# Kernel optimization log

Hardware: AMD Instinct MI355X
Metric: run time of the kernel (lower is better)

Reference implementation:

```python
import jax, jax.numpy as jnp
import numpy as np

N, NH, D, REP, C, SUB = 512, 32, 1024, 1024, 16, 64
GAMA, EPS, LN_EPS = 0.9, 1e-10, 1e-5
IMG_H, IMG_W = 800, 1280


def spatial_enc(b1, b2, h, w):
    # pocket.ops.compute_spatial_encodings: 18 handcrafted pair features + their logs -> 36
    c1x = (b1[:, 0] + b1[:, 2]) * 0.5; c1y = (b1[:, 1] + b1[:, 3]) * 0.5
    c2x = (b2[:, 0] + b2[:, 2]) * 0.5; c2y = (b2[:, 1] + b2[:, 3]) * 0.5
    b1w = b1[:, 2] - b1[:, 0]; b1h = b1[:, 3] - b1[:, 1]
    b2w = b2[:, 2] - b2[:, 0]; b2h = b2[:, 3] - b2[:, 1]
    dx = jnp.abs(c2x - c1x) / (b1w + EPS)
    dy = jnp.abs(c2y - c1y) / (b1h + EPS)
    ltx = jnp.maximum(b1[:, 0], b2[:, 0]); lty = jnp.maximum(b1[:, 1], b2[:, 1])
    rbx = jnp.minimum(b1[:, 2], b2[:, 2]); rby = jnp.minimum(b1[:, 3], b2[:, 3])
    inter = jnp.clip(rbx - ltx, 0.0) * jnp.clip(rby - lty, 0.0)
    a1 = b1w * b1h; a2 = b2w * b2h
    iou = inter / (a1 + a2 - inter)
    f = jnp.stack([
        c1x / w, c1y / h, c2x / w, c2y / h,
        b1w / w, b1h / h, b2w / w, b2h / h,
        a1 / (h * w), a2 / (h * w), a2 / (a1 + EPS),
        b1w / (b1h + EPS), b2w / (b2h + EPS), iou,
        (c2x > c1x) * dx, (c2x < c1x) * dx,
        (c2y > c1y) * dy, (c2y < c1y) * dy,
    ], axis=1)
    return jnp.concatenate([f, jnp.log(f + EPS)], axis=1)


def mbf(a, s, w1, b1, w2, b2, w3, b3):
    # relu(sum_c fc3_c(relu(fc1_c(a) * fc2_c(s)))) with branches batched over c
    u1 = jnp.einsum('pd,cdk->cpk', a, w1) + b1[:, None, :]
    u2 = jnp.einsum('ps,csk->cpk', s, w2) + b2[:, None, :]
    hdn = jax.nn.relu(u1 * u2)  # [C,P,SUB]
    out = jnp.einsum('cpk,cko->po', hdn, w3) + b3.sum(0)
    return jax.nn.relu(out)


def ln(x, g, b):
    m = x.mean(-1, keepdims=True)
    v = ((x - m) ** 2).mean(-1, keepdims=True)
    return (x - m) / jnp.sqrt(v + LN_EPS) * g + b


def setup_inputs():
    key = jax.random.key(0)
    ks = jax.random.split(key, 16)
    labels = jnp.where(jnp.arange(N) < NH, 0, 1).astype(jnp.int32)  # first NH nodes are humans
    node = jax.random.normal(ks[0], (N, D), jnp.float32)
    cx = jax.random.uniform(ks[1], (N,)) * (IMG_W * 0.5)
    cy = jax.random.uniform(ks[2], (N,)) * (IMG_H * 0.5)
    bw = jax.random.uniform(ks[3], (N,)) * (IMG_W * 0.3) + 8.0
    bh = jax.random.uniform(ks[4], (N,)) * (IMG_H * 0.3) + 8.0
    coords = jnp.stack([cx, cy, cx + bw, cy + bh], axis=1)
    p = lambda k, shp: jax.random.normal(k, shp, jnp.float32) * 0.02
    return dict(
        labels=labels, node=node, coords=coords, image_h=IMG_H, image_w=IMG_W,
        sp_w1=p(ks[5], (36, 128)), sp_b1=jnp.zeros(128),
        sp_w2=p(ks[6], (128, 256)), sp_b2=jnp.zeros(256),
        sp_w3=p(ks[7], (256, 1024)), sp_b3=jnp.zeros(1024),
        att_w1=p(ks[8], (C, 2 * D, SUB)), att_b1=jnp.zeros((C, SUB)),
        att_w2=p(ks[9], (C, 1024, SUB)), att_b2=jnp.zeros((C, SUB)),
        att_w3=p(ks[10], (C, SUB, REP)), att_b3=jnp.zeros((C, REP)),
        adj_w=p(ks[11], (REP,)), adj_b=jnp.zeros(()),
        lnh_g=jnp.ones(D), lnh_b=jnp.zeros(D),
        lno_g=jnp.ones(D), lno_b=jnp.zeros(D),
    )


def reference(labels, node, coords, image_h, image_w,
              sp_w1, sp_b1, sp_w2, sp_b2, sp_w3, sp_b3,
              att_w1, att_b1, att_w2, att_b2, att_w3, att_b3,
              adj_w, adj_b, lnh_g, lnh_b, lno_g, lno_b):
    n = node.shape[0]
    n_h = int((np.asarray(labels) == 0).sum())
    xi = np.repeat(np.arange(n_h), n)  # human index per pair
    yj = np.tile(np.arange(n), n_h)    # node index per pair
    keep = np.nonzero(xi != yj)[0]
    x = jnp.asarray(xi); y = jnp.asarray(yj)
    x_keep = jnp.asarray(xi[keep]); y_keep = jnp.asarray(yj[keep])

    f = spatial_enc(coords[x], coords[y], float(image_h), float(image_w))  # [P,36]
    sp = jax.nn.relu(f @ sp_w1 + sp_b1)
    sp = jax.nn.relu(sp @ sp_w2 + sp_b2)
    sp = jax.nn.relu(sp @ sp_w3 + sp_b3)  # [P,1024]

    human_node = node[:n_h]
    adjacency = None
    for _ in range(2):  # num_iter
        a = jnp.concatenate([human_node[x], node[y]], axis=1)  # [P,2D]
        weight = mbf(a, sp, att_w1, att_b1, att_w2, att_b2, att_w3, att_b3)  # [P,REP]
        adjacency = jax.nn.relu(weight @ adj_w + adj_b).reshape(n_h, n)
        hn_msg = adjacency @ node          # einsum('yx,xa->ya', adj, node)
        nd_msg = adjacency.T @ human_node  # einsum('yx,xa->ya', adj.T, human)
        node = ln(node * GAMA + (1.0 - GAMA) * nd_msg, lno_g, lno_b)
        human_node = ln(human_node * GAMA + (1.0 - GAMA) * hn_msg, lnh_g, lnh_b)

    return (human_node[x_keep], node[y_keep], adjacency[x_keep, y_keep], x_keep, y_keep)
```

## Files before the change

kernel.cpp:

```cpp
#include <hip/hip_runtime.h>
#include <hip/hip_bf16.h>


typedef __attribute__((ext_vector_type(4))) float  f32x4;
typedef __attribute__((ext_vector_type(8))) __bf16 bf16x8;
typedef __attribute__((ext_vector_type(4))) __bf16 bf16x4;

#define FEPS 1e-10f
#define LNEPS 1e-5f
#define GAMA_F 0.9f

__device__ __forceinline__ void gload16(const void* g, void* l) {
  __builtin_amdgcn_global_load_lds(
      (const __attribute__((address_space(1))) void*)g,
      (__attribute__((address_space(3))) void*)l, 16, 0, 0);
}

__device__ __forceinline__ float read_dim(const void* p) {
  int iv = *(const int*)p;
  if (iv > 0 && iv < (1 << 20)) return (float)iv;
  return *(const float*)p;
}

__global__ void prep_mega(const float* __restrict__ w1, const float* __restrict__ w2,
                          const float* __restrict__ w3, const float* __restrict__ spw3,
                          const float* __restrict__ spw1, const float* __restrict__ spw2,
                          const float* __restrict__ b3,
                          const float* __restrict__ node_in,
                          const float* __restrict__ coords,
                          const void* __restrict__ imh, const void* __restrict__ imw,
                          __bf16* __restrict__ W1at, __bf16* __restrict__ W1bt,
                          __bf16* __restrict__ W2t, __bf16* __restrict__ W3t,
                          __bf16* __restrict__ SpW3t,
                          __bf16* __restrict__ SpW1t, __bf16* __restrict__ SpW2t,
                          float* __restrict__ b3s,
                          float* __restrict__ node_f, __bf16* __restrict__ node_b,
                          float* __restrict__ hn_f, __bf16* __restrict__ hn_b,
                          __bf16* __restrict__ f36) {
  __shared__ float tile[64][65];
  const int b = blockIdx.x, t = threadIdx.x;
  const int tc = t & 63, tr = t >> 6;
  if (b < 256) {
    const int c = b >> 4, d0 = (b & 15) << 6;
    #pragma unroll
    for (int pass = 0; pass < 2; ++pass) {
      const float* src = w1 + (size_t)c * 131072 + (size_t)(d0 + pass * 1024) * 64;
      __bf16* dst = pass ? W1bt : W1at;
      if (pass) __syncthreads();
      #pragma unroll
      for (int q = 0; q < 16; ++q) {
        int dd = q * 4 + tr;
        tile[dd][tc] = src[dd * 64 + tc];
      }
      __syncthreads();
      #pragma unroll
      for (int q = 0; q < 16; ++q) {
        int kk = q * 4 + tr;
        dst[(size_t)(c * 64 + kk) * 1024 + d0 + tc] = (__bf16)tile[tc][kk];
      }
    }
  } else if (b < 512) {
    const int bb = b - 256, c = bb >> 4, s0 = (bb & 15) << 6;
    const float* src = w2 + (size_t)c * 65536 + (size_t)s0 * 64;
    #pragma unroll
    for (int q = 0; q < 16; ++q) {
      int ss = q * 4 + tr;
      tile[ss][tc] = src[ss * 64 + tc];
    }
    __syncthreads();
    #pragma unroll
    for (int q = 0; q < 16; ++q) {
      int kk = q * 4 + tr;
      W2t[(size_t)(c * 64 + kk) * 1024 + s0 + tc] = (__bf16)tile[tc][kk];
    }
  } else if (b < 768) {
    const int bb = b - 512, c = bb >> 4, o0 = (bb & 15) << 6;
    const float* src = w3 + (size_t)c * 65536;
    #pragma unroll
    for (int q = 0; q < 16; ++q) {
      int kk = q * 4 + tr;
      tile[kk][tc] = src[kk * 1024 + o0 + tc];
    }
    __syncthreads();
    #pragma unroll
    for (int q = 0; q < 16; ++q) {
      int oo = q * 4 + tr;
      W3t[(size_t)(o0 + oo) * 1024 + c * 64 + tc] = (__bf16)tile[tc][oo];
    }
  } else if (b < 832) {
    const int bb = b - 768, o0 = (bb >> 2) << 6, k0 = (bb & 3) << 6;
    #pragma unroll
    for (int q = 0; q < 16; ++q) {
      int kk = q * 4 + tr;
      tile[kk][tc] = spw3[(size_t)(k0 + kk) * 1024 + o0 + tc];
    }
    __syncthreads();
    #pragma unroll
    for (int q = 0; q < 16; ++q) {
      int oo = q * 4 + tr;
      SpW3t[(size_t)(o0 + oo) * 256 + k0 + tc] = (__bf16)tile[tc][oo];
    }
  } else if (b < 960) {
    int gid = (b - 832) * 256 + t;
    if (gid < 8192) {
      int n = gid >> 6, k = gid & 63;
      SpW1t[gid] = (k < 36) ? (__bf16)spw1[k * 128 + n] : (__bf16)0.f;
    }
    {
      int n = gid >> 7, k = gid & 127;
      SpW2t[gid] = (__bf16)spw2[k * 256 + n];
    }
    if (gid < 1024) {
      float s = 0.f;
      for (int cc = 0; cc < 16; ++cc) s += b3[cc * 1024 + gid];
      b3s[gid] = s;
    }
  } else if (b < 3008) {
    int gid = (b - 960) * 256 + t;
    float v = node_in[gid];
    node_f[gid] = v;
    node_b[gid] = (__bf16)v;
    if (gid < 32 * 1024) { hn_f[gid] = v; hn_b[gid] = (__bf16)v; }
  } else {
    int p = (b - 3008) * 256 + t;
    int i = p >> 9, j = p & 511;
    float H = read_dim(imh), W = read_dim(imw);
    f32x4 b1 = ((const f32x4*)coords)[i];
    f32x4 b2 = ((const f32x4*)coords)[j];
    float c1x = (b1[0] + b1[2]) * 0.5f, c1y = (b1[1] + b1[3]) * 0.5f;
    float c2x = (b2[0] + b2[2]) * 0.5f, c2y = (b2[1] + b2[3]) * 0.5f;
    float b1w = b1[2] - b1[0], b1h = b1[3] - b1[1];
    float b2w = b2[2] - b2[0], b2h = b2[3] - b2[1];
    float dx = fabsf(c2x - c1x) / (b1w + FEPS);
    float dy = fabsf(c2y - c1y) / (b1h + FEPS);
    float ltx = fmaxf(b1[0], b2[0]), lty = fmaxf(b1[1], b2[1]);
    float rbx = fminf(b1[2], b2[2]), rby = fminf(b1[3], b2[3]);
    float inter = fmaxf(rbx - ltx, 0.f) * fmaxf(rby - lty, 0.f);
    float a1 = b1w * b1h, a2 = b2w * b2h;
    float iou = inter / (a1 + a2 - inter);
    float f[18];
    f[0] = c1x / W;  f[1] = c1y / H;  f[2] = c2x / W;  f[3] = c2y / H;
    f[4] = b1w / W;  f[5] = b1h / H;  f[6] = b2w / W;  f[7] = b2h / H;
    f[8] = a1 / (H * W); f[9] = a2 / (H * W); f[10] = a2 / (a1 + FEPS);
    f[11] = b1w / (b1h + FEPS); f[12] = b2w / (b2h + FEPS); f[13] = iou;
    f[14] = (c2x > c1x) ? dx : 0.f; f[15] = (c2x < c1x) ? dx : 0.f;
    f[16] = (c2y > c1y) ? dy : 0.f; f[17] = (c2y < c1y) ? dy : 0.f;
    __bf16 o[64];
    #pragma unroll
    for (int q = 0; q < 18; ++q) { o[q] = (__bf16)f[q]; o[18 + q] = (__bf16)logf(f[q] + FEPS); }
    #pragma unroll
    for (int q = 36; q < 64; ++q) o[q] = (__bf16)0.f;
    bf16x8* dst = (bf16x8*)(f36 + (size_t)p * 64);
    #pragma unroll
    for (int q = 0; q < 8; ++q) dst[q] = *(bf16x8*)&o[q * 8];
  }
}

__global__ __launch_bounds__(256)
void mlp_head(const __bf16* __restrict__ f36, const __bf16* __restrict__ SpW1t,
              const __bf16* __restrict__ SpW2t, const float* __restrict__ b1,
              const float* __restrict__ b2, __bf16* __restrict__ sp2out) {
  __shared__ __align__(16) __bf16 Af[128 * 64];
  __shared__ __align__(16) __bf16 W1s[128 * 64];
  __shared__ __align__(16) __bf16 S1[128 * 128];
  __shared__ __align__(16) __bf16 W2s[256 * 128];
  const int t = threadIdx.x;
  const int lane = t & 63, wv = t >> 6;
  const int wr = wv >> 1, wc = wv & 1;
  const int lr = lane & 15, lg = lane >> 4;
  const int m0 = blockIdx.x * 128;

  #pragma unroll
  for (int cc = 0; cc < 4; ++cc)
    gload16(f36 + (size_t)m0 * 64 + (wv * 4 + cc) * 512 + lane * 8, &Af[(wv * 4 + cc) * 512 + lane * 8]);
  #pragma unroll
  for (int cc = 0; cc < 4; ++cc)
    gload16(SpW1t + (wv * 4 + cc) * 512 + lane * 8, &W1s[(wv * 4 + cc) * 512 + lane * 8]);
  #pragma unroll
  for (int cc = 0; cc < 16; ++cc)
    gload16(SpW2t + (wv * 16 + cc) * 512 + lane * 8, &W2s[(wv * 16 + cc) * 512 + lane * 8]);
  __syncthreads();

  {
    f32x4 acc[4][4] = {};
    #pragma unroll
    for (int ks = 0; ks < 2; ++ks) {
      bf16x8 af[4], bf[4];
      #pragma unroll
      for (int mi = 0; mi < 4; ++mi)
        af[mi] = *(const bf16x8*)&Af[(wr * 64 + mi * 16 + lr) * 64 + ks * 32 + lg * 8];
      #pragma unroll
      for (int ni = 0; ni < 4; ++ni)
        bf[ni] = *(const bf16x8*)&W1s[(wc * 64 + ni * 16 + lr) * 64 + ks * 32 + lg * 8];
      #pragma unroll
      for (int mi = 0; mi < 4; ++mi)
        #pragma unroll
        for (int ni = 0; ni < 4; ++ni)
          acc[mi][ni] = __builtin_amdgcn_mfma_f32_16x16x32_bf16(af[mi], bf[ni], acc[mi][ni], 0, 0, 0);
    }
    __syncthreads();
    #pragma unroll
    for (int mi = 0; mi < 4; ++mi)
      #pragma unroll
      for (int r = 0; r < 4; ++r) {
        int R = wr * 64 + mi * 16 + lg * 4 + r;
        #pragma unroll
        for (int ni = 0; ni < 4; ++ni) {
          int Cc = wc * 64 + ni * 16 + lr;
          S1[R * 128 + Cc] = (__bf16)fmaxf(acc[mi][ni][r] + b1[Cc], 0.f);
        }
      }
  }
  __syncthreads();

  {
    f32x4 acc[4][8] = {};
    #pragma unroll
    for (int ks = 0; ks < 4; ++ks) {
      bf16x8 af[4];
      #pragma unroll
      for (int mi = 0; mi < 4; ++mi)
        af[mi] = *(const bf16x8*)&S1[(wr * 64 + mi * 16 + lr) * 128 + ks * 32 + lg * 8];
      #pragma unroll
      for (int ni = 0; ni < 8; ++ni) {
        bf16x8 bf = *(const bf16x8*)&W2s[(wc * 128 + ni * 16 + lr) * 128 + ks * 32 + lg * 8];
        #pragma unroll
        for (int mi = 0; mi < 4; ++mi)
          acc[mi][ni] = __builtin_amdgcn_mfma_f32_16x16x32_bf16(af[mi], bf, acc[mi][ni], 0, 0, 0);
      }
    }
    #pragma unroll
    for (int mi = 0; mi < 4; ++mi)
      #pragma unroll
      for (int r = 0; r < 4; ++r) {
        int R = m0 + wr * 64 + mi * 16 + lg * 4 + r;
        #pragma unroll
        for (int ni = 0; ni < 8; ++ni) {
          int Cc = wc * 128 + ni * 16 + lr;
          sp2out[(size_t)R * 256 + Cc] = (__bf16)fmaxf(acc[mi][ni][r] + b2[Cc], 0.f);
        }
      }
  }
}

template <int EPI>
__global__ __launch_bounds__(256)
void gemm_bt(const __bf16* __restrict__ A, const __bf16* __restrict__ Bt,
             const float* __restrict__ bias, void* __restrict__ C,
             int M, int N, int K) {
  __shared__ __align__(16) __bf16 As[128 * 64];
  __shared__ __align__(16) __bf16 Bs[128 * 64];
  const int t = threadIdx.x;
  const int lane = t & 63, wv = t >> 6;
  const int wr = wv >> 1, wc = wv & 1;
  const int lr = lane & 15, lg = lane >> 4;
  const int lrow = lane >> 3, lcol = (lane & 7) << 3;
  const int m0 = blockIdx.x * 128, n0 = blockIdx.y * 128;

  f32x4 acc[4][4] = {};
  const int nkt = K >> 6;
  for (int kt = 0; kt < nkt; ++kt) {
    const int k0 = kt << 6;
    #pragma unroll
    for (int it = 0; it < 4; ++it) {
      const int rbase = wv * 32 + it * 8;
      gload16(A + (size_t)(m0 + rbase + lrow) * K + k0 + lcol, &As[rbase * 64]);
      gload16(Bt + (size_t)(n0 + rbase + lrow) * K + k0 + lcol, &Bs[rbase * 64]);
    }
    __syncthreads();
    #pragma unroll
    for (int ks = 0; ks < 2; ++ks) {
      bf16x8 af[4], bfr[4];
      #pragma unroll
      for (int mi = 0; mi < 4; ++mi)
        af[mi] = *(const bf16x8*)&As[(wr * 64 + mi * 16 + lr) * 64 + ks * 32 + lg * 8];
      #pragma unroll
      for (int ni = 0; ni < 4; ++ni)
        bfr[ni] = *(const bf16x8*)&Bs[(wc * 64 + ni * 16 + lr) * 64 + ks * 32 + lg * 8];
      #pragma unroll
      for (int mi = 0; mi < 4; ++mi)
        #pragma unroll
        for (int ni = 0; ni < 4; ++ni)
          acc[mi][ni] = __builtin_amdgcn_mfma_f32_16x16x32_bf16(af[mi], bfr[ni], acc[mi][ni], 0, 0, 0);
    }
    __syncthreads();
  }
  #pragma unroll
  for (int mi = 0; mi < 4; ++mi)
    #pragma unroll
    for (int r = 0; r < 4; ++r) {
      int R = m0 + wr * 64 + mi * 16 + lg * 4 + r;
      #pragma unroll
      for (int ni = 0; ni < 4; ++ni) {
        int Cc = n0 + wc * 64 + ni * 16 + lr;
        float v = acc[mi][ni][r] + bias[Cc];
        if constexpr (EPI == 0) v = fmaxf(v, 0.f);
        ((__bf16*)C)[(size_t)R * N + Cc] = (__bf16)v;
      }
    }
}

__global__ __launch_bounds__(256)
void u1hdn(const __bf16* __restrict__ hn_b, const __bf16* __restrict__ node_b,
           const __bf16* __restrict__ W1at, const __bf16* __restrict__ W1bt,
           const float* __restrict__ b1, const __bf16* __restrict__ u2,
           __bf16* __restrict__ hdn) {
  __shared__ __align__(16) __bf16 AsH[32 * 64];
  __shared__ __align__(16) __bf16 AsN[32 * 64];
  __shared__ __align__(16) __bf16 BsH[128 * 64];
  __shared__ __align__(16) __bf16 BsN[128 * 64];
  const int t = threadIdx.x;
  const int lane = t & 63, wv = t >> 6;
  const int lr = lane & 15, lg = lane >> 4;
  const int lrow = lane >> 3, lcol = (lane & 7) << 3;
  const int j0 = blockIdx.x * 32;
  const int n0 = blockIdx.y * 128;
  const bool isH = wv < 2;
  const int r0 = (wv & 1) * 16;

  f32x4 acc[8] = {};
  for (int kt = 0; kt < 16; ++kt) {
    const int k0 = kt << 6;
    gload16(hn_b + (size_t)(wv * 8 + lrow) * 1024 + k0 + lcol, &AsH[(wv * 8) * 64]);
    gload16(node_b + (size_t)(j0 + wv * 8 + lrow) * 1024 + k0 + lcol, &AsN[(wv * 8) * 64]);
    #pragma unroll
    for (int it = 0; it < 4; ++it) {
      const int rbase = wv * 32 + it * 8;
      gload16(W1at + (size_t)(n0 + rbase + lrow) * 1024 + k0 + lcol, &BsH[rbase * 64]);
      gload16(W1bt + (size_t)(n0 + rbase + lrow) * 1024 + k0 + lcol, &BsN[rbase * 64]);
    }
    __syncthreads();
    const __bf16* Asrc = isH ? AsH : AsN;
    const __bf16* Bsrc = isH ? BsH : BsN;
    #pragma unroll
    for (int ks = 0; ks < 2; ++ks) {
      bf16x8 af = *(const bf16x8*)&Asrc[(r0 + lr) * 64 + ks * 32 + lg * 8];
      #pragma unroll
      for (int ni = 0; ni < 8; ++ni) {
        bf16x8 bfr = *(const bf16x8*)&Bsrc[(ni * 16 + lr) * 64 + ks * 32 + lg * 8];
        acc[ni] = __builtin_amdgcn_mfma_f32_16x16x32_bf16(af, bfr, acc[ni], 0, 0, 0);
      }
    }
    __syncthreads();
  }

  float* H1s = (float*)BsH;
  float* N1s = (float*)BsN;
  #pragma unroll
  for (int ni = 0; ni < 8; ++ni)
    #pragma unroll
    for (int r = 0; r < 4; ++r) {
      int row = r0 + lg * 4 + r;
      int col = ni * 16 + lr;
      float v = acc[ni][r];
      if (isH) H1s[row * 128 + col] = v + b1[n0 + col];
      else     N1s[row * 128 + col] = v;
    }
  __syncthreads();

  const int rsub = t >> 4, csub = (t & 15) * 8;
  for (int pass = 0; pass < 64; ++pass) {
    int rp = pass * 16 + rsub;
    int i = rp >> 5, jl = rp & 31;
    size_t p = (size_t)i * 512 + j0 + jl;
    bf16x8 u = *(const bf16x8*)(u2 + p * 1024 + n0 + csub);
    const float* hp = &H1s[i * 128 + csub];
    const float* np = &N1s[jl * 128 + csub];
    bf16x8 o;
    #pragma unroll
    for (int e = 0; e < 8; ++e)
      o[e] = (__bf16)fmaxf((hp[e] + np[e]) * (float)u[e], 0.f);
    *(bf16x8*)(hdn + p * 1024 + n0 + csub) = o;
  }
}

__global__ __launch_bounds__(256)
void gemm_adj(const __bf16* __restrict__ hdn, const __bf16* __restrict__ W3t,
              const float* __restrict__ b3s, const float* __restrict__ adjw,
              float* __restrict__ adjpre8) {
  __shared__ __align__(16) __bf16 As[128 * 64];
  __shared__ __align__(16) __bf16 Bs[128 * 64];
  __shared__ float redbuf[2][128];
  const int t = threadIdx.x;
  const int lane = t & 63, wv = t >> 6;
  const int wr = wv >> 1, wc = wv & 1;
  const int lr = lane & 15, lg = lane >> 4;
  const int lrow = lane >> 3, lcol = (lane & 7) << 3;
  const int m0 = blockIdx.x * 128;
  const int h = blockIdx.y, c0 = h * 128;

  f32x4 acc[4][4] = {};
  for (int kt = 0; kt < 16; ++kt) {
    const int k0 = kt << 6;
    #pragma unroll
    for (int it = 0; it < 4; ++it) {
      const int rbase = wv * 32 + it * 8;
      gload16(hdn + (size_t)(m0 + rbase + lrow) * 1024 + k0 + lcol, &As[rbase * 64]);
      gload16(W3t + (size_t)(c0 + rbase + lrow) * 1024 + k0 + lcol, &Bs[rbase * 64]);
    }
    __syncthreads();
    #pragma unroll
    for (int ks = 0; ks < 2; ++ks) {
      bf16x8 af[4], bfr[4];
      #pragma unroll
      for (int mi = 0; mi < 4; ++mi)
        af[mi] = *(const bf16x8*)&As[(wr * 64 + mi * 16 + lr) * 64 + ks * 32 + lg * 8];
      #pragma unroll
      for (int ni = 0; ni < 4; ++ni)
        bfr[ni] = *(const bf16x8*)&Bs[(wc * 64 + ni * 16 + lr) * 64 + ks * 32 + lg * 8];
      #pragma unroll
      for (int mi = 0; mi < 4; ++mi)
        #pragma unroll
        for (int ni = 0; ni < 4; ++ni)
          acc[mi][ni] = __builtin_amdgcn_mfma_f32_16x16x32_bf16(af[mi], bfr[ni], acc[mi][ni], 0, 0, 0);
    }
    __syncthreads();
  }

  float b3v[4], awv[4];
  #pragma unroll
  for (int ni = 0; ni < 4; ++ni) {
    int Cc = c0 + wc * 64 + ni * 16 + lr;
    b3v[ni] = b3s[Cc];
    awv[ni] = adjw[Cc];
  }
  #pragma unroll
  for (int mi = 0; mi < 4; ++mi)
    #pragma unroll
    for (int r = 0; r < 4; ++r) {
      float s = 0.f;
      #pragma unroll
      for (int ni = 0; ni < 4; ++ni)
        s += fmaxf(acc[mi][ni][r] + b3v[ni], 0.f) * awv[ni];
      s += __shfl_xor(s, 1);
      s += __shfl_xor(s, 2);
      s += __shfl_xor(s, 4);
      s += __shfl_xor(s, 8);
      if (lr == 0)
        redbuf[wc][wr * 64 + mi * 16 + lg * 4 + r] = s;
    }
  __syncthreads();
  if (t < 128)
    adjpre8[(size_t)h * 16384 + m0 + t] = redbuf[0][t] + redbuf[1][t];
}

__global__ void msgln(const float* __restrict__ adjpre8, const float* __restrict__ adjb,
                      const float* __restrict__ node_in_f, const float* __restrict__ hn_in_f,
                      const float* __restrict__ lno_g, const float* __restrict__ lno_b,
                      const float* __restrict__ lnh_g, const float* __restrict__ lnh_b,
                      float* __restrict__ node_out_f, float* __restrict__ hn_out_f,
                      __bf16* __restrict__ node_bb, __bf16* __restrict__ hn_bb) {
  __shared__ float adjrow[512];
  __shared__ float sbuf[4];
  const int row = blockIdx.x, t = threadIdx.x;
  const float ab = adjb[0];
  const bool isH = row < 32;
  f32x4 msg = {0.f, 0.f, 0.f, 0.f};
  if (isH) {
    const int i = row;
    float s0 = 0.f, s1 = 0.f;
    #pragma unroll
    for (int h = 0; h < 8; ++h) {
      s0 += adjpre8[(size_t)h * 16384 + i * 512 + t];
      s1 += adjpre8[(size_t)h * 16384 + i * 512 + 256 + t];
    }
    adjrow[t] = fmaxf(s0 + ab, 0.f);
    adjrow[256 + t] = fmaxf(s1 + ab, 0.f);
    __syncthreads();
    for (int j = 0; j < 512; ++j)
      msg += adjrow[j] * ((const f32x4*)node_in_f)[j * 256 + t];
  } else {
    const int j = row - 32;
    int i = t >> 3, hh = t & 7;
    float v = adjpre8[(size_t)hh * 16384 + i * 512 + j];
    v += __shfl_xor(v, 1);
    v += __shfl_xor(v, 2);
    v += __shfl_xor(v, 4);
    if (hh == 0) adjrow[i] = fmaxf(v + ab, 0.f);
    __syncthreads();
    for (int i2 = 0; i2 < 32; ++i2)
      msg += adjrow[i2] * ((const f32x4*)hn_in_f)[i2 * 256 + t];
  }
  const int r = isH ? row : row - 32;
  const float* X = (isH ? hn_in_f : node_in_f) + (size_t)r * 1024;
  const float* g = isH ? lnh_g : lno_g;
  const float* bb = isH ? lnh_b : lno_b;
  float* Xo = (isH ? hn_out_f : node_out_f) + (size_t)r * 1024;
  __bf16* Xb = (isH ? hn_bb : node_bb) + (size_t)r * 1024;

  f32x4 x = ((const f32x4*)X)[t];
  f32x4 y;
  #pragma unroll
  for (int e = 0; e < 4; ++e) y[e] = x[e] * GAMA_F + (1.0f - GAMA_F) * msg[e];
  float s = y[0] + y[1] + y[2] + y[3];
  #pragma unroll
  for (int mm = 32; mm >= 1; mm >>= 1) s += __shfl_xor(s, mm);
  if ((t & 63) == 0) sbuf[t >> 6] = s;
  __syncthreads();
  float mean = (sbuf[0] + sbuf[1] + sbuf[2] + sbuf[3]) * (1.0f / 1024.0f);
  __syncthreads();
  f32x4 d;
  #pragma unroll
  for (int e = 0; e < 4; ++e) d[e] = y[e] - mean;
  float sq = d[0] * d[0] + d[1] * d[1] + d[2] * d[2] + d[3] * d[3];
  #pragma unroll
  for (int mm = 32; mm >= 1; mm >>= 1) sq += __shfl_xor(sq, mm);
  if ((t & 63) == 0) sbuf[t >> 6] = sq;
  __syncthreads();
  float var = (sbuf[0] + sbuf[1] + sbuf[2] + sbuf[3]) * (1.0f / 1024.0f);
  float inv = rsqrtf(var + LNEPS);
  f32x4 gg = ((const f32x4*)g)[t];
  f32x4 bv = ((const f32x4*)bb)[t];
  f32x4 o;
  bf16x4 ob;
  #pragma unroll
  for (int e = 0; e < 4; ++e) { o[e] = d[e] * inv * gg[e] + bv[e]; ob[e] = (__bf16)o[e]; }
  ((f32x4*)Xo)[t] = o;
  *(bf16x4*)(Xb + t * 4) = ob;
}

__global__ void gather_k(const float* __restrict__ hn, const float* __restrict__ node,
                         const float* __restrict__ adjpre8, const float* __restrict__ adjb,
                         float* __restrict__ out) {
  int p = blockIdx.x, t = threadIdx.x;
  int i = p >> 9, j = p & 511;
  if (i == j) return;
  int m = p - (p + 512) / 513;
  float* out0 = out;
  float* out1 = out + (size_t)16352 * 1024;
  float* out2 = out1 + (size_t)16352 * 1024;
  ((f32x4*)out0)[(size_t)m * 256 + t] = ((const f32x4*)hn)[i * 256 + t];
  ((f32x4*)out1)[(size_t)m * 256 + t] = ((const f32x4*)node)[j * 256 + t];
  if (t == 0) {
    float s = adjb[0];
    #pragma unroll
    for (int h = 0; h < 8; ++h) s += adjpre8[(size_t)h * 16384 + p];
    out2[m] = fmaxf(s, 0.f);
    out2[16352 + m] = (float)i;
    out2[2 * 16352 + m] = (float)j;
  }
}

extern "C" void kernel_launch(void* const* d_in, const int* in_sizes, int n_in,
                              void* d_out, int out_size, void* d_ws, size_t ws_size,
                              hipStream_t stream) {
  const float* node_in = (const float*)d_in[1];
  const float* coords  = (const float*)d_in[2];
  const void*  imh     = d_in[3];
  const void*  imw     = d_in[4];
  const float* sp_w1 = (const float*)d_in[5];
  const float* sp_b1 = (const float*)d_in[6];
  const float* sp_w2 = (const float*)d_in[7];
  const float* sp_b2 = (const float*)d_in[8];
  const float* sp_w3 = (const float*)d_in[9];
  const float* sp_b3 = (const float*)d_in[10];
  const float* att_w1 = (const float*)d_in[11];
  const float* att_b1 = (const float*)d_in[12];
  const float* att_w2 = (const float*)d_in[13];
  const float* att_b2 = (const float*)d_in[14];
  const float* att_w3 = (const float*)d_in[15];
  const float* att_b3 = (const float*)d_in[16];
  const float* adj_w  = (const float*)d_in[17];
  const float* adj_b  = (const float*)d_in[18];
  const float* lnh_g  = (const float*)d_in[19];
  const float* lnh_b  = (const float*)d_in[20];
  const float* lno_g  = (const float*)d_in[21];
  const float* lno_b  = (const float*)d_in[22];

  char* w = (char*)d_ws;
  size_t off = 0;
  auto alloc = [&](size_t bytes) -> char* {
    char* p = w + off;
    off += (bytes + 255) & ~(size_t)255;
    return p;
  };
  __bf16* W1at  = (__bf16*)alloc((size_t)1024 * 1024 * 2);
  __bf16* W1bt  = (__bf16*)alloc((size_t)1024 * 1024 * 2);
  __bf16* W2t   = (__bf16*)alloc((size_t)1024 * 1024 * 2);
  __bf16* W3t   = (__bf16*)alloc((size_t)1024 * 1024 * 2);
  __bf16* SpW1t = (__bf16*)alloc(128 * 64 * 2);
  __bf16* SpW2t = (__bf16*)alloc(256 * 128 * 2);
  __bf16* SpW3t = (__bf16*)alloc(1024 * 256 * 2);
  float*  b3s   = (float*)alloc(1024 * 4);
  __bf16* f36   = (__bf16*)alloc((size_t)16384 * 64 * 2);
  __bf16* sp2   = (__bf16*)alloc((size_t)16384 * 256 * 2);
  __bf16* spb   = (__bf16*)alloc((size_t)16384 * 1024 * 2);
  __bf16* u2    = (__bf16*)alloc((size_t)16384 * 1024 * 2);
  float*  adjpre8 = (float*)alloc((size_t)8 * 16384 * 4);
  float*  node_f0 = (float*)alloc((size_t)512 * 1024 * 4);
  float*  node_f1 = (float*)alloc((size_t)512 * 1024 * 4);
  float*  hn_f0   = (float*)alloc((size_t)32 * 1024 * 4);
  float*  hn_f1   = (float*)alloc((size_t)32 * 1024 * 4);
  __bf16* node_b  = (__bf16*)alloc((size_t)512 * 1024 * 2);
  __bf16* hn_b    = (__bf16*)alloc((size_t)32 * 1024 * 2);
  if (off > ws_size) return;

  prep_mega<<<3072, 256, 0, stream>>>(att_w1, att_w2, att_w3, sp_w3, sp_w1, sp_w2, att_b3,
                                      node_in, coords, imh, imw,
                                      W1at, W1bt, W2t, W3t, SpW3t, SpW1t, SpW2t, b3s,
                                      node_f0, node_b, hn_f0, hn_b, f36);
  mlp_head<<<128, 256, 0, stream>>>(f36, SpW1t, SpW2t, sp_b1, sp_b2, sp2);
  gemm_bt<0><<<dim3(128, 8), 256, 0, stream>>>(sp2, SpW3t, sp_b3, spb, 16384, 1024, 256);
  gemm_bt<1><<<dim3(128, 8), 256, 0, stream>>>(spb, W2t, att_b2, u2, 16384, 1024, 1024);

  __bf16* hdn = spb;
  u1hdn<<<dim3(16, 8), 256, 0, stream>>>(hn_b, node_b, W1at, W1bt, att_b1, u2, hdn);
  gemm_adj<<<dim3(128, 8), 256, 0, stream>>>(hdn, W3t, b3s, adj_w, adjpre8);
  msgln<<<544, 256, 0, stream>>>(adjpre8, adj_b, node_f0, hn_f0,
                                 lno_g, lno_b, lnh_g, lnh_b,
                                 node_f1, hn_f1, node_b, hn_b);
  u1hdn<<<dim3(16, 8), 256, 0, stream>>>(hn_b, node_b, W1at, W1bt, att_b1, u2, hdn);
  gemm_adj<<<dim3(128, 8), 256, 0, stream>>>(hdn, W3t, b3s, adj_w, adjpre8);
  msgln<<<544, 256, 0, stream>>>(adjpre8, adj_b, node_f1, hn_f1,
                                 lno_g, lno_b, lnh_g, lnh_b,
                                 node_f0, hn_f0, node_b, hn_b);

  gather_k<<<16384, 256, 0, stream>>>(hn_f0, node_f0, adjpre8, adj_b, (float*)d_out);
}
```

Baseline: 547.6 us.

## Split u1hdn into GEMM plus elementwise kernel, remap GEMM blocks per XCD, shrink mlp_head tiles

The fused u1hdn kernel ran on only 128 blocks and wrote the 32 MB hdn tensor inside a serial loop. It is replaced by a small gemm_u1 that writes H1 and N1 in fp32 and a fully parallel build_hdn elementwise kernel with 8192 blocks. The gemm_bt and gemm_adj kernels now use a 1D grid whose block index is remapped so that consecutive blocks on the same XCD share M rows, which should improve L2 reuse. mlp_head uses 64-row tiles to launch twice as many blocks and reads its weights directly from global memory instead of staging them in LDS. The split adds an extra launch and an fp32 intermediate round trip through memory.

```diff
diff --git a/kernel.cpp b/kernel.cpp
--- a/kernel.cpp
+++ b/kernel.cpp
@@ -160,50 +160,40 @@
 void mlp_head(const __bf16* __restrict__ f36, const __bf16* __restrict__ SpW1t,
               const __bf16* __restrict__ SpW2t, const float* __restrict__ b1,
               const float* __restrict__ b2, __bf16* __restrict__ sp2out) {
-  __shared__ __align__(16) __bf16 Af[128 * 64];
-  __shared__ __align__(16) __bf16 W1s[128 * 64];
-  __shared__ __align__(16) __bf16 S1[128 * 128];
-  __shared__ __align__(16) __bf16 W2s[256 * 128];
+  __shared__ __align__(16) __bf16 Af[64 * 64];
+  __shared__ __align__(16) __bf16 S1[64 * 128];
   const int t = threadIdx.x;
   const int lane = t & 63, wv = t >> 6;
   const int wr = wv >> 1, wc = wv & 1;
   const int lr = lane & 15, lg = lane >> 4;
-  const int m0 = blockIdx.x * 128;
-
-  #pragma unroll
-  for (int cc = 0; cc < 4; ++cc)
-    gload16(f36 + (size_t)m0 * 64 + (wv * 4 + cc) * 512 + lane * 8, &Af[(wv * 4 + cc) * 512 + lane * 8]);
-  #pragma unroll
-  for (int cc = 0; cc < 4; ++cc)
-    gload16(SpW1t + (wv * 4 + cc) * 512 + lane * 8, &W1s[(wv * 4 + cc) * 512 + lane * 8]);
-  #pragma unroll
-  for (int cc = 0; cc < 16; ++cc)
-    gload16(SpW2t + (wv * 16 + cc) * 512 + lane * 8, &W2s[(wv * 16 + cc) * 512 + lane * 8]);
+  const int m0 = blockIdx.x * 64;
+
+  gload16(f36 + (size_t)m0 * 64 + t * 16, &Af[t * 16]);
+  gload16(f36 + (size_t)m0 * 64 + 4096 + t * 8, &Af[4096 + t * 8]);
   __syncthreads();
 
   {
-    f32x4 acc[4][4] = {};
+    f32x4 acc[2][4] = {};
     #pragma unroll
     for (int ks = 0; ks < 2; ++ks) {
-      bf16x8 af[4], bf[4];
-      #pragma unroll
-      for (int mi = 0; mi < 4; ++mi)
-        af[mi] = *(const bf16x8*)&Af[(wr * 64 + mi * 16 + lr) * 64 + ks * 32 + lg * 8];
+      bf16x8 af[2], bf[4];
+      #pragma unroll
+      for (int mi = 0; mi < 2; ++mi)
+        af[mi] = *(const bf16x8*)&Af[(wr * 32 + mi * 16 + lr) * 64 + ks * 32 + lg * 8];
       #pragma unroll
       for (int ni = 0; ni < 4; ++ni)
-        bf[ni] = *(const bf16x8*)&W1s[(wc * 64 + ni * 16 + lr) * 64 + ks * 32 + lg * 8];
-      #pragma unroll
-      for (int mi = 0; mi < 4; ++mi)
+        bf[ni] = *(const bf16x8*)(SpW1t + (size_t)(wc * 64 + ni * 16 + lr) * 64 + ks * 32 + lg * 8);
+      #pragma unroll
+      for (int mi = 0; mi < 2; ++mi)
         #pragma unroll
         for (int ni = 0; ni < 4; ++ni)
           acc[mi][ni] = __builtin_amdgcn_mfma_f32_16x16x32_bf16(af[mi], bf[ni], acc[mi][ni], 0, 0, 0);
     }
-    __syncthreads();
-    #pragma unroll
-    for (int mi = 0; mi < 4; ++mi)
+    #pragma unroll
+    for (int mi = 0; mi < 2; ++mi)
       #pragma unroll
       for (int r = 0; r < 4; ++r) {
-        int R = wr * 64 + mi * 16 + lg * 4 + r;
+        int R = wr * 32 + mi * 16 + lg * 4 + r;
         #pragma unroll
         for (int ni = 0; ni < 4; ++ni) {
           int Cc = wc * 64 + ni * 16 + lr;
@@ -214,26 +204,26 @@
   __syncthreads();
 
   {
-    f32x4 acc[4][8] = {};
+    f32x4 acc[2][8] = {};
     #pragma unroll
     for (int ks = 0; ks < 4; ++ks) {
-      bf16x8 af[4];
-      #pragma unroll
-      for (int mi = 0; mi < 4; ++mi)
-        af[mi] = *(const bf16x8*)&S1[(wr * 64 + mi * 16 + lr) * 128 + ks * 32 + lg * 8];
+      bf16x8 af[2];
+      #pragma unroll
+      for (int mi = 0; mi < 2; ++mi)
+        af[mi] = *(const bf16x8*)&S1[(wr * 32 + mi * 16 + lr) * 128 + ks * 32 + lg * 8];
       #pragma unroll
       for (int ni = 0; ni < 8; ++ni) {
-        bf16x8 bf = *(const bf16x8*)&W2s[(wc * 128 + ni * 16 + lr) * 128 + ks * 32 + lg * 8];
+        bf16x8 bf = *(const bf16x8*)(SpW2t + (size_t)(wc * 128 + ni * 16 + lr) * 128 + ks * 32 + lg * 8);
         #pragma unroll
-        for (int mi = 0; mi < 4; ++mi)
+        for (int mi = 0; mi < 2; ++mi)
           acc[mi][ni] = __builtin_amdgcn_mfma_f32_16x16x32_bf16(af[mi], bf, acc[mi][ni], 0, 0, 0);
       }
     }
     #pragma unroll
-    for (int mi = 0; mi < 4; ++mi)
+    for (int mi = 0; mi < 2; ++mi)
       #pragma unroll
       for (int r = 0; r < 4; ++r) {
-        int R = m0 + wr * 64 + mi * 16 + lg * 4 + r;
+        int R = m0 + wr * 32 + mi * 16 + lg * 4 + r;
         #pragma unroll
         for (int ni = 0; ni < 8; ++ni) {
           int Cc = wc * 128 + ni * 16 + lr;
@@ -247,7 +237,7 @@
 __global__ __launch_bounds__(256)
 void gemm_bt(const __bf16* __restrict__ A, const __bf16* __restrict__ Bt,
              const float* __restrict__ bias, void* __restrict__ C,
-             int M, int N, int K) {
+             int N, int K) {
   __shared__ __align__(16) __bf16 As[128 * 64];
   __shared__ __align__(16) __bf16 Bs[128 * 64];
   const int t = threadIdx.x;
@@ -255,7 +245,10 @@
   const int wr = wv >> 1, wc = wv & 1;
   const int lr = lane & 15, lg = lane >> 4;
   const int lrow = lane >> 3, lcol = (lane & 7) << 3;
-  const int m0 = blockIdx.x * 128, n0 = blockIdx.y * 128;
+  const int b = blockIdx.x;
+  const int xcd = b & 7, seq = b >> 3;
+  const int m0 = (xcd * 16 + (seq >> 3)) * 128;
+  const int n0 = (seq & 7) * 128;
 
   f32x4 acc[4][4] = {};
   const int nkt = K >> 6;
@@ -301,77 +294,71 @@
 }
 
 __global__ __launch_bounds__(256)
-void u1hdn(const __bf16* __restrict__ hn_b, const __bf16* __restrict__ node_b,
-           const __bf16* __restrict__ W1at, const __bf16* __restrict__ W1bt,
-           const float* __restrict__ b1, const __bf16* __restrict__ u2,
-           __bf16* __restrict__ hdn) {
-  __shared__ __align__(16) __bf16 AsH[32 * 64];
-  __shared__ __align__(16) __bf16 AsN[32 * 64];
-  __shared__ __align__(16) __bf16 BsH[128 * 64];
-  __shared__ __align__(16) __bf16 BsN[128 * 64];
+void gemm_u1(const __bf16* __restrict__ hn_b, const __bf16* __restrict__ node_b,
+             const __bf16* __restrict__ W1at, const __bf16* __restrict__ W1bt,
+             const float* __restrict__ b1, float* __restrict__ H1, float* __restrict__ N1) {
+  __shared__ __align__(16) __bf16 As[32 * 64];
+  __shared__ __align__(16) __bf16 Bs[128 * 64];
   const int t = threadIdx.x;
   const int lane = t & 63, wv = t >> 6;
+  const int wr = wv >> 1, wc = wv & 1;
   const int lr = lane & 15, lg = lane >> 4;
   const int lrow = lane >> 3, lcol = (lane & 7) << 3;
-  const int j0 = blockIdx.x * 32;
+  const bool isH = (blockIdx.x == 0);
+  const __bf16* Ap = isH ? hn_b : node_b + (size_t)(blockIdx.x - 1) * 32 * 1024;
+  const __bf16* Bp = isH ? W1at : W1bt;
   const int n0 = blockIdx.y * 128;
-  const bool isH = wv < 2;
-  const int r0 = (wv & 1) * 16;
-
-  f32x4 acc[8] = {};
+
+  f32x4 acc[4] = {};
   for (int kt = 0; kt < 16; ++kt) {
     const int k0 = kt << 6;
-    gload16(hn_b + (size_t)(wv * 8 + lrow) * 1024 + k0 + lcol, &AsH[(wv * 8) * 64]);
-    gload16(node_b + (size_t)(j0 + wv * 8 + lrow) * 1024 + k0 + lcol, &AsN[(wv * 8) * 64]);
+    gload16(Ap + (size_t)(wv * 8 + lrow) * 1024 + k0 + lcol, &As[(wv * 8) * 64]);
     #pragma unroll
     for (int it = 0; it < 4; ++it) {
       const int rbase = wv * 32 + it * 8;
-      gload16(W1at + (size_t)(n0 + rbase + lrow) * 1024 + k0 + lcol, &BsH[rbase * 64]);
-      gload16(W1bt + (size_t)(n0 + rbase + lrow) * 1024 + k0 + lcol, &BsN[rbase * 64]);
-    }
-    __syncthreads();
-    const __bf16* Asrc = isH ? AsH : AsN;
-    const __bf16* Bsrc = isH ? BsH : BsN;
+      gload16(Bp + (size_t)(n0 + rbase + lrow) * 1024 + k0 + lcol, &Bs[rbase * 64]);
+    }
+    __syncthreads();
     #pragma unroll
     for (int ks = 0; ks < 2; ++ks) {
-      bf16x8 af = *(const bf16x8*)&Asrc[(r0 + lr) * 64 + ks * 32 + lg * 8];
-      #pragma unroll
-      for (int ni = 0; ni < 8; ++ni) {
-        bf16x8 bfr = *(const bf16x8*)&Bsrc[(ni * 16 + lr) * 64 + ks * 32 + lg * 8];
+      bf16x8 af = *(const bf16x8*)&As[(wr * 16 + lr) * 64 + ks * 32 + lg * 8];
+      #pragma unroll
+      for (int ni = 0; ni < 4; ++ni) {
+        bf16x8 bfr = *(const bf16x8*)&Bs[(wc * 64 + ni * 16 + lr) * 64 + ks * 32 + lg * 8];
         acc[ni] = __builtin_amdgcn_mfma_f32_16x16x32_bf16(af, bfr, acc[ni], 0, 0, 0);
       }
     }
     __syncthreads();
   }
-
-  float* H1s = (float*)BsH;
-  float* N1s = (float*)BsN;
-  #pragma unroll
-  for (int ni = 0; ni < 8; ++ni)
+  #pragma unroll
+  for (int ni = 0; ni < 4; ++ni)
     #pragma unroll
     for (int r = 0; r < 4; ++r) {
-      int row = r0 + lg * 4 + r;
-      int col = ni * 16 + lr;
+      int R = wr * 16 + lg * 4 + r;
+      int Cc = n0 + wc * 64 + ni * 16 + lr;
       float v = acc[ni][r];
-      if (isH) H1s[row * 128 + col] = v + b1[n0 + col];
-      else     N1s[row * 128 + col] = v;
-    }
-  __syncthreads();
-
-  const int rsub = t >> 4, csub = (t & 15) * 8;
-  for (int pass = 0; pass < 64; ++pass) {
-    int rp = pass * 16 + rsub;
-    int i = rp >> 5, jl = rp & 31;
-    size_t p = (size_t)i * 512 + j0 + jl;
-    bf16x8 u = *(const bf16x8*)(u2 + p * 1024 + n0 + csub);
-    const float* hp = &H1s[i * 128 + csub];
-    const float* np = &N1s[jl * 128 + csub];
-    bf16x8 o;
-    #pragma unroll
-    for (int e = 0; e < 8; ++e)
-      o[e] = (__bf16)fmaxf((hp[e] + np[e]) * (float)u[e], 0.f);
-    *(bf16x8*)(hdn + p * 1024 + n0 + csub) = o;
-  }
+      if (isH) H1[(size_t)R * 1024 + Cc] = v + b1[Cc];
+      else     N1[((size_t)(blockIdx.x - 1) * 32 + R) * 1024 + Cc] = v;
+    }
+}
+
+__global__ void build_hdn(const __bf16* __restrict__ u2, const float* __restrict__ H1,
+                          const float* __restrict__ N1, __bf16* __restrict__ hdn) {
+  int gid = blockIdx.x * 256 + threadIdx.x;
+  int p = gid >> 7, c8 = (gid & 127) << 3;
+  int i = p >> 9, j = p & 511;
+  bf16x8 u = *(const bf16x8*)(u2 + (size_t)p * 1024 + c8);
+  const float* hp = H1 + (size_t)i * 1024 + c8;
+  const float* np = N1 + (size_t)j * 1024 + c8;
+  f32x4 h0 = *(const f32x4*)hp, h1 = *(const f32x4*)(hp + 4);
+  f32x4 n0 = *(const f32x4*)np, n1 = *(const f32x4*)(np + 4);
+  bf16x8 o;
+  #pragma unroll
+  for (int e = 0; e < 4; ++e) {
+    o[e]     = (__bf16)fmaxf((h0[e] + n0[e]) * (float)u[e], 0.f);
+    o[4 + e] = (__bf16)fmaxf((h1[e] + n1[e]) * (float)u[4 + e], 0.f);
+  }
+  *(bf16x8*)(hdn + (size_t)p * 1024 + c8) = o;
 }
 
 __global__ __launch_bounds__(256)
@@ -386,8 +373,10 @@
   const int wr = wv >> 1, wc = wv & 1;
   const int lr = lane & 15, lg = lane >> 4;
   const int lrow = lane >> 3, lcol = (lane & 7) << 3;
-  const int m0 = blockIdx.x * 128;
-  const int h = blockIdx.y, c0 = h * 128;
+  const int b = blockIdx.x;
+  const int xcd = b & 7, seq = b >> 3;
+  const int m0 = (xcd * 16 + (seq >> 3)) * 128;
+  const int h = seq & 7, c0 = h * 128;
 
   f32x4 acc[4][4] = {};
   for (int kt = 0; kt < 16; ++kt) {
@@ -586,6 +575,8 @@
   __bf16* sp2   = (__bf16*)alloc((size_t)16384 * 256 * 2);
   __bf16* spb   = (__bf16*)alloc((size_t)16384 * 1024 * 2);
   __bf16* u2    = (__bf16*)alloc((size_t)16384 * 1024 * 2);
+  float*  H1    = (float*)alloc((size_t)32 * 1024 * 4);
+  float*  N1    = (float*)alloc((size_t)512 * 1024 * 4);
   float*  adjpre8 = (float*)alloc((size_t)8 * 16384 * 4);
   float*  node_f0 = (float*)alloc((size_t)512 * 1024 * 4);
   float*  node_f1 = (float*)alloc((size_t)512 * 1024 * 4);
@@ -599,18 +590,20 @@
                                       node_in, coords, imh, imw,
                                       W1at, W1bt, W2t, W3t, SpW3t, SpW1t, SpW2t, b3s,
                                       node_f0, node_b, hn_f0, hn_b, f36);
-  mlp_head<<<128, 256, 0, stream>>>(f36, SpW1t, SpW2t, sp_b1, sp_b2, sp2);
-  gemm_bt<0><<<dim3(128, 8), 256, 0, stream>>>(sp2, SpW3t, sp_b3, spb, 16384, 1024, 256);
-  gemm_bt<1><<<dim3(128, 8), 256, 0, stream>>>(spb, W2t, att_b2, u2, 16384, 1024, 1024);
+  mlp_head<<<256, 256, 0, stream>>>(f36, SpW1t, SpW2t, sp_b1, sp_b2, sp2);
+  gemm_bt<0><<<1024, 256, 0, stream>>>(sp2, SpW3t, sp_b3, spb, 1024, 256);
+  gemm_bt<1><<<1024, 256, 0, stream>>>(spb, W2t, att_b2, u2, 1024, 1024);
 
   __bf16* hdn = spb;
-  u1hdn<<<dim3(16, 8), 256, 0, stream>>>(hn_b, node_b, W1at, W1bt, att_b1, u2, hdn);
-  gemm_adj<<<dim3(128, 8), 256, 0, stream>>>(hdn, W3t, b3s, adj_w, adjpre8);
+  gemm_u1<<<dim3(17, 8), 256, 0, stream>>>(hn_b, node_b, W1at, W1bt, att_b1, H1, N1);
+  build_hdn<<<8192, 256, 0, stream>>>(u2, H1, N1, hdn);
+  gemm_adj<<<1024, 256, 0, stream>>>(hdn, W3t, b3s, adj_w, adjpre8);
   msgln<<<544, 256, 0, stream>>>(adjpre8, adj_b, node_f0, hn_f0,
                                  lno_g, lno_b, lnh_g, lnh_b,
                                  node_f1, hn_f1, node_b, hn_b);
-  u1hdn<<<dim3(16, 8), 256, 0, stream>>>(hn_b, node_b, W1at, W1bt, att_b1, u2, hdn);
-  gemm_adj<<<dim3(128, 8), 256, 0, stream>>>(hdn, W3t, b3s, adj_w, adjpre8);
+  gemm_u1<<<dim3(17, 8), 256, 0, stream>>>(hn_b, node_b, W1at, W1bt, att_b1, H1, N1);
+  build_hdn<<<8192, 256, 0, stream>>>(u2, H1, N1, hdn);
+  gemm_adj<<<1024, 256, 0, stream>>>(hdn, W3t, b3s, adj_w, adjpre8);
   msgln<<<544, 256, 0, stream>>>(adjpre8, adj_b, node_f1, hn_f1,
                                  lno_g, lno_b, lnh_g, lnh_b,
                                  node_f0, hn_f0, node_b, hn_b);
```

Result: faster. 501.4 us (-8.4%).
